# Performance work log

Hardware: AMD Instinct MI355X
Metric: run time of the kernel (lower is better)

The kernel has to match this reference:

```python
import jax, jax.numpy as jnp
import numpy as np

B, S, D = 4, 1024, 4096
HQ, HKV = 32, 8
HD = D // HQ          # 128
SCALE = HQ // HKV     # 4 (GQA repeat factor)


def setup_inputs() -> dict:
    key = jax.random.key(0)
    ks = jax.random.split(key, 11)
    s = 0.02  # init scale for weights
    return {
        "x": jax.random.normal(ks[0], (B, S, D), jnp.float32),
        # freqs_cis stored as (real, imag) pairs: [S, HD//2, 2]
        "freqs_cis": jax.random.normal(ks[1], (S, HD // 2, 2), jnp.float32),
        "Wq": jax.random.normal(ks[2], (D, HQ * HD), jnp.float32) * s,
        "bq": jnp.zeros((HQ * HD,), jnp.float32),
        "Wk": jax.random.normal(ks[3], (D, HKV * HD), jnp.float32) * s,
        "bk": jnp.zeros((HKV * HD,), jnp.float32),
        "Wv": jax.random.normal(ks[4], (D, HKV * HD), jnp.float32) * s,
        "bv": jnp.zeros((HKV * HD,), jnp.float32),
        "Wo": jax.random.normal(ks[5], (D, D), jnp.float32) * s,
        "bo": jnp.zeros((D,), jnp.float32),
        "startpos": 0,
    }


def _apply_rotary(x, fc):
    # x: [B, S, H, HD]; fc: [S, HD//2, 2] (real, imag)
    xr = x.reshape(*x.shape[:-1], HD // 2, 2)
    a, b = xr[..., 0], xr[..., 1]
    c = fc[None, :, None, :, 0]  # [1, S, 1, HD//2]
    d = fc[None, :, None, :, 1]
    # complex multiply (a+ib)*(c+id)
    out = jnp.stack([a * c - b * d, a * d + b * c], axis=-1)
    return out.reshape(x.shape)


def reference(x, freqs_cis, Wq, bq, Wk, bk, Wv, bv, Wo, bo, startpos):
    b, s, _ = x.shape
    q = (x @ Wq + bq).reshape(b, s, HQ, HD)
    k = (x @ Wk + bk).reshape(b, s, HKV, HD)
    v = (x @ Wv + bv).reshape(b, s, HKV, HD)

    fc = freqs_cis[startpos:startpos + s]
    q = _apply_rotary(q, fc)
    k = _apply_rotary(k, fc)

    # startpos == 0 and seq == cache_seq: cache write/read is identity
    q = q.transpose(0, 2, 1, 3)                            # [b, HQ, s, HD]
    k = jnp.repeat(k.transpose(0, 2, 1, 3), SCALE, axis=1)  # GQA repeat -> [b, HQ, s, HD]
    v = jnp.repeat(v.transpose(0, 2, 1, 3), SCALE, axis=1)

    scores = jnp.einsum('bhqd,bhkd->bhqk', q, k) / jnp.sqrt(jnp.float32(HD))
    causal = jnp.tril(jnp.ones((s, s), bool))
    scores = jnp.where(causal, scores, -jnp.inf)
    attn = jax.nn.softmax(scores, axis=-1)
    o = jnp.einsum('bhqk,bhkd->bhqd', attn, v)
    o = o.transpose(0, 2, 1, 3).reshape(b, s, HQ * HD)
    return o @ Wo + bo
```

## Files before the change

kernel.cpp:

```cpp
#include <hip/hip_runtime.h>
#include <hip/hip_bf16.h>

using bf16x8   = __attribute__((ext_vector_type(8))) __bf16;
using floatx4  = __attribute__((ext_vector_type(4))) float;
using floatx16 = __attribute__((ext_vector_type(16))) float;

#define DEVINL __device__ __forceinline__

DEVINL void gload16(const void* g, void* l) {
  __builtin_amdgcn_global_load_lds(
      (__attribute__((address_space(1))) void*)g,
      (__attribute__((address_space(3))) void*)l,
      16, 0, 0);
}

constexpr int S_ = 1024, D_ = 4096, HQ_ = 32, HKV_ = 8, HD_ = 128, B_ = 4;

__global__ void conv_bf16(const float* __restrict__ in, __bf16* __restrict__ out, int n) {
  int i = (blockIdx.x * 256 + threadIdx.x) * 8;
  if (i >= n) return;
  float4 a = *(const float4*)(in + i);
  float4 b = *(const float4*)(in + i + 4);
  bf16x8 o;
  o[0] = (__bf16)a.x; o[1] = (__bf16)a.y; o[2] = (__bf16)a.z; o[3] = (__bf16)a.w;
  o[4] = (__bf16)b.x; o[5] = (__bf16)b.y; o[6] = (__bf16)b.z; o[7] = (__bf16)b.w;
  *(bf16x8*)(out + i) = o;
}

__global__ void conv_transpose(const float* __restrict__ W, __bf16* __restrict__ WT, int K, int N) {
  __shared__ float tile[32][33];
  int n0 = blockIdx.x * 32, k0 = blockIdx.y * 32;
  int tx = threadIdx.x & 31, ty = threadIdx.x >> 5;
#pragma unroll
  for (int i = 0; i < 32; i += 8)
    tile[ty + i][tx] = W[(size_t)(k0 + ty + i) * N + n0 + tx];
  __syncthreads();
#pragma unroll
  for (int i = 0; i < 32; i += 8)
    WT[(size_t)(n0 + ty + i) * K + k0 + tx] = (__bf16)tile[tx][ty + i];
}

template<int MODE>
__global__ __launch_bounds__(512, 2)
void gemm8(const __bf16* __restrict__ A, const __bf16* __restrict__ BT,
           const float* __restrict__ b0, const float* __restrict__ b1,
           const float* __restrict__ b2, void* __restrict__ Cout,
           int M, int N, int K)
{
  __shared__ __bf16 lds[49152];
  const int t = threadIdx.x;
  const int lane = t & 63, w = t >> 6;
  const int wm = w >> 2, wn = w & 3;
  const int g = lane >> 4, c = lane & 15;

  const int gridX = gridDim.x;
  const int nwg = gridDim.x * gridDim.y;
  int lin = blockIdx.y * gridDim.x + blockIdx.x;
  lin = (lin & 7) * (nwg >> 3) + (lin >> 3);
  const int bx = lin % gridX, by = lin / gridX;
  const int m0 = by * 128, n0 = bx * 256;

  const floatx4 zero4 = {0.f, 0.f, 0.f, 0.f};
  floatx4 acc[4][4];
#pragma unroll
  for (int i = 0; i < 4; i++)
#pragma unroll
    for (int j = 0; j < 4; j++) acc[i][j] = zero4;

  const int arow = t >> 2;
  const int achk = (t & 3) ^ ((t >> 3) & 3);
  const __bf16* Ag  = A  + (size_t)(m0 + arow) * K + achk * 8;
  const __bf16* Bg0 = BT + (size_t)(n0 + arow) * K + achk * 8;
  const __bf16* Bg1 = BT + (size_t)(n0 + arow + 128) * K + achk * 8;

  const int sl = (g ^ ((c >> 1) & 3)) * 8;
  const int abase = (wm * 64 + c) * 32 + sl;
  const int bbase = 4096 + (wn * 64 + c) * 32 + sl;

  const int NT = K >> 5;

  auto STAGE = [&](int kt) {
    const int buf = (kt & 3) * 12288;
    const size_t ko = (size_t)kt * 32;
    gload16(Ag  + ko, &lds[buf + t * 8]);
    gload16(Bg0 + ko, &lds[buf + 4096 + t * 8]);
    gload16(Bg1 + ko, &lds[buf + 8192 + t * 8]);
  };

  STAGE(0);
  STAGE(1);
  asm volatile("s_waitcnt vmcnt(3)" ::: "memory");
  __builtin_amdgcn_s_barrier();
  __builtin_amdgcn_sched_barrier(0);

  for (int kt = 0; kt < NT; ++kt) {
    const int buf = (kt & 3) * 12288;
    bf16x8 af[4], bfr[4];
#pragma unroll
    for (int i = 0; i < 4; i++)
      af[i] = *(const bf16x8*)&lds[buf + abase + i * 512];
#pragma unroll
    for (int j = 0; j < 4; j++)
      bfr[j] = *(const bf16x8*)&lds[buf + bbase + j * 512];
    if (kt + 2 < NT) STAGE(kt + 2);
    __builtin_amdgcn_sched_barrier(0);
    __builtin_amdgcn_s_barrier();
    __builtin_amdgcn_sched_barrier(0);
    __builtin_amdgcn_s_setprio(1);
#pragma unroll
    for (int i = 0; i < 4; i++)
#pragma unroll
      for (int j = 0; j < 4; j++)
        acc[i][j] = __builtin_amdgcn_mfma_f32_16x16x32_bf16(af[i], bfr[j], acc[i][j], 0, 0, 0);
    __builtin_amdgcn_s_setprio(0);
    __builtin_amdgcn_sched_barrier(0);
    if (kt + 2 < NT) { asm volatile("s_waitcnt vmcnt(3)" ::: "memory"); }
    else             { asm volatile("s_waitcnt vmcnt(0)" ::: "memory"); }
    __builtin_amdgcn_s_barrier();
    __builtin_amdgcn_sched_barrier(0);
  }

#pragma unroll
  for (int j = 0; j < 4; j++) {
    const int ncol = n0 + wn * 64 + j * 16 + c;
#pragma unroll
    for (int i = 0; i < 4; i++) {
      const int mbase = m0 + wm * 64 + i * 16 + g * 4;
#pragma unroll
      for (int r = 0; r < 4; r++) {
        const int m = mbase + r;
        float v = acc[i][j][r];
        if constexpr (MODE == 0) {
          ((float*)Cout)[(size_t)m * N + ncol] = v + b0[ncol];
        } else {
          const int bb = m >> 10, s = m & 1023;
          __bf16* qkv = (__bf16*)Cout;
          if (ncol < 4096) {
            v += b0[ncol];
            const int h = ncol >> 7, d = ncol & 127;
            qkv[(((size_t)bb * 32 + h) * 1024 + s) * 128 + d] = (__bf16)v;
          } else if (ncol < 5120) {
            const int nc = ncol - 4096;
            v += b1[nc];
            const int h = nc >> 7, d = nc & 127;
            qkv[16777216 + (((size_t)bb * 8 + h) * 1024 + s) * 128 + d] = (__bf16)v;
          } else {
            const int nc = ncol - 5120;
            v += b2[nc];
            const int h = nc >> 7, d = nc & 127;
            qkv[20971520 + (((size_t)bb * 8 + h) * 128 + d) * 1024 + s] = (__bf16)v;
          }
        }
      }
    }
  }
}

constexpr int NQCH = B_ * HQ_ * S_ * (HD_ / 8);
constexpr int NKCH = B_ * HKV_ * S_ * (HD_ / 8);
__global__ void rope_kernel(__bf16* __restrict__ qt, __bf16* __restrict__ kt,
                            const float* __restrict__ fc, const int* __restrict__ sp) {
  int tid = blockIdx.x * 256 + threadIdx.x;
  __bf16* p;
  int idx;
  if (tid < NQCH) { p = qt; idx = tid; }
  else { idx = tid - NQCH; if (idx >= NKCH) return; p = kt; }
  const int c8 = idx & 15;
  const int s  = (idx >> 4) & 1023;
  const int srow = sp[0] + s;
  const float* f = fc + (size_t)srow * 128 + c8 * 8;
  float4 fa = *(const float4*)(f);
  float4 fb = *(const float4*)(f + 4);
  __bf16* q = p + (size_t)idx * 8;
  bf16x8 v = *(const bf16x8*)q;
  float a0 = (float)v[0], b0 = (float)v[1], a1 = (float)v[2], b1 = (float)v[3];
  float a2 = (float)v[4], b2 = (float)v[5], a3 = (float)v[6], b3 = (float)v[7];
  bf16x8 o;
  o[0] = (__bf16)(a0 * fa.x - b0 * fa.y); o[1] = (__bf16)(a0 * fa.y + b0 * fa.x);
  o[2] = (__bf16)(a1 * fa.z - b1 * fa.w); o[3] = (__bf16)(a1 * fa.w + b1 * fa.z);
  o[4] = (__bf16)(a2 * fb.x - b2 * fb.y); o[5] = (__bf16)(a2 * fb.y + b2 * fb.x);
  o[6] = (__bf16)(a3 * fb.z - b3 * fb.w); o[7] = (__bf16)(a3 * fb.w + b3 * fb.z);
  *(bf16x8*)q = o;
}

__global__ __launch_bounds__(256, 2)
void flash_attn(const __bf16* __restrict__ qt, const __bf16* __restrict__ kt,
                const __bf16* __restrict__ vt, __bf16* __restrict__ obuf)
{
  const int lane = threadIdx.x & 63, w = threadIdx.x >> 6;
  const int rl = lane & 31, hi = lane >> 5;
  const int qb = blockIdx.x & 7;
  const int bh = blockIdx.x >> 3;
  const int b = bh >> 5, h = bh & 31, hk = h >> 2;
  const int q0w = (qb + w * 8) * 32;

  const __bf16* Qp = qt + (size_t)(b * HQ_ + h) * S_ * HD_;
  const __bf16* Kp = kt + (size_t)(b * HKV_ + hk) * S_ * HD_;
  const __bf16* Vp = vt + (size_t)(b * HKV_ + hk) * HD_ * S_;

  const __bf16* Qb = Qp + (size_t)(q0w + rl) * HD_ + hi * 8;
  bf16x8 qf[8];
#pragma unroll
  for (int d = 0; d < 8; d++) qf[d] = *(const bf16x8*)(Qb + d * 16);

  const __bf16* Kb = Kp + (size_t)rl * HD_ + hi * 8;
  const __bf16* Vb = Vp + (size_t)rl * S_ + hi * 8;

  const floatx16 zero16 = {0.f,0.f,0.f,0.f,0.f,0.f,0.f,0.f,0.f,0.f,0.f,0.f,0.f,0.f,0.f,0.f};
  floatx16 oacc[4];
#pragma unroll
  for (int dt = 0; dt < 4; dt++) oacc[dt] = zero16;

  float m_run = -__builtin_inff();
  float l_run = 0.f;
  const float ksc = 0.12751744875895f;

  for (int kv0 = 0; kv0 <= q0w; kv0 += 32) {
    floatx16 acc = zero16;
    bf16x8 kf[8];
#pragma unroll
    for (int d = 0; d < 8; d++)
      kf[d] = *(const bf16x8*)(Kb + (size_t)kv0 * HD_ + d * 16);
#pragma unroll
    for (int d = 0; d < 8; d++)
      acc = __builtin_amdgcn_mfma_f32_32x32x16_bf16(kf[d], qf[d], acc, 0, 0, 0);

    bf16x8 vf[4][2];
#pragma unroll
    for (int dt = 0; dt < 4; dt++)
#pragma unroll
      for (int kh = 0; kh < 2; kh++)
        vf[dt][kh] = *(const bf16x8*)(Vb + (size_t)dt * 32 * S_ + kv0 + kh * 16);

    if (kv0 == q0w) {
#pragma unroll
      for (int r = 0; r < 16; r++) {
        const int krel = (r & 3) + 8 * (r >> 2) + 4 * hi;
        if (krel > rl) acc[r] = -3e29f;
      }
    }

    float mx = acc[0];
#pragma unroll
    for (int r = 1; r < 16; r++) mx = fmaxf(mx, acc[r]);
    mx = fmaxf(mx, __shfl_xor(mx, 32));
    const float m_cand = mx * ksc;

    float m_use;
    const bool defer = __all(m_cand - m_run <= 8.0f);
    if (defer) {
      m_use = m_run;
    } else {
      const float m_new = fmaxf(m_run, m_cand);
      const float alpha = exp2f(m_run - m_new);
      l_run *= alpha;
      float ar[16];
#pragma unroll
      for (int r = 0; r < 16; r++)
        ar[r] = __shfl(alpha, (r & 3) + 8 * (r >> 2) + 4 * hi);
#pragma unroll
      for (int dt = 0; dt < 4; dt++)
#pragma unroll
        for (int r = 0; r < 16; r++) oacc[dt][r] *= ar[r];
      m_run = m_new;
      m_use = m_new;
    }

    float pr[16];
#pragma unroll
    for (int r = 0; r < 16; r++) pr[r] = exp2f(fmaf(acc[r], ksc, -m_use));
    float rs = pr[0];
#pragma unroll
    for (int r = 1; r < 16; r++) rs += pr[r];
    rs += __shfl_xor(rs, 32);
    l_run += rs;

    bf16x8 pa[2];
#pragma unroll
    for (int kh = 0; kh < 2; kh++) {
      const int rb = kh * 8;
      unsigned a0, b0, a1, b1;
      asm("v_cvt_pk_bf16_f32 %0, %1, %2" : "=v"(a0) : "v"(pr[rb + 0]), "v"(pr[rb + 1]));
      asm("v_cvt_pk_bf16_f32 %0, %1, %2" : "=v"(b0) : "v"(pr[rb + 4]), "v"(pr[rb + 5]));
      asm("v_cvt_pk_bf16_f32 %0, %1, %2" : "=v"(a1) : "v"(pr[rb + 2]), "v"(pr[rb + 3]));
      asm("v_cvt_pk_bf16_f32 %0, %1, %2" : "=v"(b1) : "v"(pr[rb + 6]), "v"(pr[rb + 7]));
      asm("v_permlane32_swap_b32 %0, %1" : "+v"(a0), "+v"(b0));
      asm("v_permlane32_swap_b32 %0, %1" : "+v"(a1), "+v"(b1));
      union { unsigned u[4]; bf16x8 v; } cvt;
      cvt.u[0] = a0; cvt.u[1] = a1; cvt.u[2] = b0; cvt.u[3] = b1;
      pa[kh] = cvt.v;
    }

#pragma unroll
    for (int dt = 0; dt < 4; dt++) {
      oacc[dt] = __builtin_amdgcn_mfma_f32_32x32x16_bf16(pa[0], vf[dt][0], oacc[dt], 0, 0, 0);
      oacc[dt] = __builtin_amdgcn_mfma_f32_32x32x16_bf16(pa[1], vf[dt][1], oacc[dt], 0, 0, 0);
    }
  }

  const float linv = 1.f / l_run;
  float lr[16];
#pragma unroll
  for (int r = 0; r < 16; r++)
    lr[r] = __shfl(linv, (r & 3) + 8 * (r >> 2) + 4 * hi);
#pragma unroll
  for (int dt = 0; dt < 4; dt++)
#pragma unroll
    for (int r = 0; r < 16; r++) {
      const int qrow = q0w + (r & 3) + 8 * (r >> 2) + 4 * hi;
      const size_t o = (size_t)(b * S_ + qrow) * D_ + h * HD_ + dt * 32 + rl;
      obuf[o] = (__bf16)(oacc[dt][r] * lr[r]);
    }
}

extern "C" void kernel_launch(void* const* d_in, const int* in_sizes, int n_in,
                              void* d_out, int out_size, void* d_ws, size_t ws_size,
                              hipStream_t stream) {
  (void)in_sizes; (void)n_in; (void)out_size;
  const float* x  = (const float*)d_in[0];
  const float* fc = (const float*)d_in[1];
  const float* Wq = (const float*)d_in[2];
  const float* bq = (const float*)d_in[3];
  const float* Wk = (const float*)d_in[4];
  const float* bk = (const float*)d_in[5];
  const float* Wv = (const float*)d_in[6];
  const float* bv = (const float*)d_in[7];
  const float* Wo = (const float*)d_in[8];
  const float* bo = (const float*)d_in[9];
  const int*   sp = (const int*)d_in[10];
  float* out = (float*)d_out;

  const size_t MB = 1024 * 1024;
  if (ws_size < 192 * MB) return;
  char* ws = (char*)d_ws;
  __bf16* xb     = (__bf16*)(ws + 0);
  __bf16* WqkvT  = (__bf16*)(ws + 32 * MB);
  __bf16* WoT    = (__bf16*)(ws + 80 * MB);
  __bf16* q_t    = (__bf16*)(ws + 112 * MB);
  __bf16* k_t    = (__bf16*)(ws + 144 * MB);
  __bf16* v_t    = (__bf16*)(ws + 152 * MB);
  __bf16* ob     = (__bf16*)(ws + 160 * MB);

  conv_bf16<<<8192, 256, 0, stream>>>(x, xb, D_ * B_ * S_);
  conv_transpose<<<dim3(128, 128), 256, 0, stream>>>(Wq, WqkvT, 4096, 4096);
  conv_transpose<<<dim3(32, 128),  256, 0, stream>>>(Wk, WqkvT + (size_t)4096 * 4096, 4096, 1024);
  conv_transpose<<<dim3(32, 128),  256, 0, stream>>>(Wv, WqkvT + (size_t)5120 * 4096, 4096, 1024);
  conv_transpose<<<dim3(128, 128), 256, 0, stream>>>(Wo, WoT, 4096, 4096);

  gemm8<1><<<dim3(24, 32), 512, 0, stream>>>(xb, WqkvT, bq, bk, bv, q_t, 4096, 6144, 4096);

  rope_kernel<<<(NQCH + NKCH) / 256, 256, 0, stream>>>(q_t, k_t, fc, sp);
  flash_attn<<<1024, 256, 0, stream>>>(q_t, k_t, v_t, ob);

  gemm8<0><<<dim3(16, 32), 512, 0, stream>>>(ob, WoT, bo, nullptr, nullptr, out, 4096, 4096, 4096);
}
```

Before: 664.3 us.

## Enlarge GEMM tiles to 256x256 with quadrant-pipelined double-buffered K=64 loads

Replaces the 128x256 GEMM with a 256x256 tile kernel using BK=64 and two LDS buffers. Each K step is split into four quadrant phases, each staging one 128-row sub-tile of the next stage while MFMAs run on the current one, with staggered vmcnt waits. The larger tile raises arithmetic intensity per global byte. In exchange it uses 128KB of LDS per block, which limits occupancy, and it halves the grid: 384 and 256 blocks spread across the device's CUs.

```diff
diff --git a/kernel.cpp b/kernel.cpp
--- a/kernel.cpp
+++ b/kernel.cpp
@@ -42,118 +42,170 @@
 
 template<int MODE>
 __global__ __launch_bounds__(512, 2)
-void gemm8(const __bf16* __restrict__ A, const __bf16* __restrict__ BT,
-           const float* __restrict__ b0, const float* __restrict__ b1,
-           const float* __restrict__ b2, void* __restrict__ Cout,
-           int M, int N, int K)
+void gemm8p(const __bf16* __restrict__ A, const __bf16* __restrict__ BT,
+            const float* __restrict__ b0, const float* __restrict__ b1,
+            const float* __restrict__ b2, void* __restrict__ Cout,
+            int M, int N, int K)
 {
-  __shared__ __bf16 lds[49152];
+  __shared__ __bf16 lds[65536];
   const int t = threadIdx.x;
   const int lane = t & 63, w = t >> 6;
   const int wm = w >> 2, wn = w & 3;
-  const int g = lane >> 4, c = lane & 15;
+  const int g = (lane >> 4) & 3, c = lane & 15;
 
   const int gridX = gridDim.x;
   const int nwg = gridDim.x * gridDim.y;
   int lin = blockIdx.y * gridDim.x + blockIdx.x;
   lin = (lin & 7) * (nwg >> 3) + (lin >> 3);
   const int bx = lin % gridX, by = lin / gridX;
-  const int m0 = by * 128, n0 = bx * 256;
+  const int m0 = by * 256, n0 = bx * 256;
 
   const floatx4 zero4 = {0.f, 0.f, 0.f, 0.f};
-  floatx4 acc[4][4];
-#pragma unroll
-  for (int i = 0; i < 4; i++)
-#pragma unroll
-    for (int j = 0; j < 4; j++) acc[i][j] = zero4;
-
-  const int arow = t >> 2;
-  const int achk = (t & 3) ^ ((t >> 3) & 3);
-  const __bf16* Ag  = A  + (size_t)(m0 + arow) * K + achk * 8;
-  const __bf16* Bg0 = BT + (size_t)(n0 + arow) * K + achk * 8;
-  const __bf16* Bg1 = BT + (size_t)(n0 + arow + 128) * K + achk * 8;
-
-  const int sl = (g ^ ((c >> 1) & 3)) * 8;
-  const int abase = (wm * 64 + c) * 32 + sl;
-  const int bbase = 4096 + (wn * 64 + c) * 32 + sl;
-
-  const int NT = K >> 5;
-
-  auto STAGE = [&](int kt) {
-    const int buf = (kt & 3) * 12288;
-    const size_t ko = (size_t)kt * 32;
-    gload16(Ag  + ko, &lds[buf + t * 8]);
-    gload16(Bg0 + ko, &lds[buf + 4096 + t * 8]);
-    gload16(Bg1 + ko, &lds[buf + 8192 + t * 8]);
-  };
-
-  STAGE(0);
-  STAGE(1);
-  asm volatile("s_waitcnt vmcnt(3)" ::: "memory");
-  __builtin_amdgcn_s_barrier();
+  floatx4 acc[2][2][4][2];
+#pragma unroll
+  for (int a = 0; a < 2; a++)
+#pragma unroll
+    for (int bq = 0; bq < 2; bq++)
+#pragma unroll
+      for (int i = 0; i < 4; i++)
+#pragma unroll
+        for (int j = 0; j < 2; j++) acc[a][bq][i][j] = zero4;
+
+  const int t3 = t >> 3;
+  const int l8 = ((t & 7) ^ (t3 & 7)) * 8;
+  const int browc = (t3 & 31) + ((t3 >> 5) << 6);
+  const __bf16* srcA0 = A  + (size_t)(m0 + t3) * K + l8;
+  const __bf16* srcA1 = A  + (size_t)(m0 + 64 + t3) * K + l8;
+  const __bf16* srcB0 = BT + (size_t)(n0 + browc) * K + l8;
+  const __bf16* srcB1 = BT + (size_t)(n0 + 32 + browc) * K + l8;
+  const size_t k128 = (size_t)128 * K;
+
+  const int arow_rd = (wm * 64 + c) * 64;
+  const int brow_rd = (wn * 32 + c) * 64;
+  const int sel0 = ((g) ^ (c & 7)) * 8;
+  const int sel1 = ((4 + g) ^ (c & 7)) * 8;
+
+  const int NT = K >> 6;
+
+#define STG(srcp, subofs, kt, pbuf)                                              \
+  gload16((srcp) + (size_t)(kt) * 64,        &lds[(pbuf) + (subofs) + t * 8]);   \
+  gload16((srcp) + (size_t)(kt) * 64 + k128, &lds[(pbuf) + (subofs) + 4096 + t * 8]);
+
+#define LOADA(MQ, bb)                                                            \
+  _Pragma("unroll")                                                              \
+  for (int i = 0; i < 4; i++) {                                                  \
+    af[i][0] = *(const bf16x8*)&lds[(bb) + (MQ)*8192 + arow_rd + i*1024 + sel0]; \
+    af[i][1] = *(const bf16x8*)&lds[(bb) + (MQ)*8192 + arow_rd + i*1024 + sel1]; \
+  }
+
+#define LOADB(NQ, bb)                                                            \
+  _Pragma("unroll")                                                              \
+  for (int j = 0; j < 2; j++) {                                                  \
+    bf[j][0] = *(const bf16x8*)&lds[(bb) + 16384 + (NQ)*8192 + brow_rd + j*1024 + sel0]; \
+    bf[j][1] = *(const bf16x8*)&lds[(bb) + 16384 + (NQ)*8192 + brow_rd + j*1024 + sel1]; \
+  }
+
+#define MFMAQ(MQ, NQ)                                                            \
+  __builtin_amdgcn_s_setprio(1);                                                 \
+  _Pragma("unroll")                                                              \
+  for (int i = 0; i < 4; i++)                                                    \
+    _Pragma("unroll")                                                            \
+    for (int j = 0; j < 2; j++) {                                                \
+      acc[MQ][NQ][i][j] = __builtin_amdgcn_mfma_f32_16x16x32_bf16(af[i][0], bf[j][0], acc[MQ][NQ][i][j], 0, 0, 0); \
+      acc[MQ][NQ][i][j] = __builtin_amdgcn_mfma_f32_16x16x32_bf16(af[i][1], bf[j][1], acc[MQ][NQ][i][j], 0, 0, 0); \
+    }                                                                            \
+  __builtin_amdgcn_s_setprio(0);                                                 \
   __builtin_amdgcn_sched_barrier(0);
 
-  for (int kt = 0; kt < NT; ++kt) {
-    const int buf = (kt & 3) * 12288;
-    bf16x8 af[4], bfr[4];
-#pragma unroll
-    for (int i = 0; i < 4; i++)
-      af[i] = *(const bf16x8*)&lds[buf + abase + i * 512];
-#pragma unroll
-    for (int j = 0; j < 4; j++)
-      bfr[j] = *(const bf16x8*)&lds[buf + bbase + j * 512];
-    if (kt + 2 < NT) STAGE(kt + 2);
-    __builtin_amdgcn_sched_barrier(0);
-    __builtin_amdgcn_s_barrier();
-    __builtin_amdgcn_sched_barrier(0);
-    __builtin_amdgcn_s_setprio(1);
-#pragma unroll
-    for (int i = 0; i < 4; i++)
-#pragma unroll
-      for (int j = 0; j < 4; j++)
-        acc[i][j] = __builtin_amdgcn_mfma_f32_16x16x32_bf16(af[i], bfr[j], acc[i][j], 0, 0, 0);
-    __builtin_amdgcn_s_setprio(0);
-    __builtin_amdgcn_sched_barrier(0);
-    if (kt + 2 < NT) { asm volatile("s_waitcnt vmcnt(3)" ::: "memory"); }
-    else             { asm volatile("s_waitcnt vmcnt(0)" ::: "memory"); }
-    __builtin_amdgcn_s_barrier();
-    __builtin_amdgcn_sched_barrier(0);
+#define BAR()                                                                    \
+  __builtin_amdgcn_sched_barrier(0);                                             \
+  __builtin_amdgcn_s_barrier();                                                  \
+  __builtin_amdgcn_sched_barrier(0);
+
+#define VMC(N) asm volatile("s_waitcnt vmcnt(" #N ")" ::: "memory");
+
+#define TILE(v, DOSTAGE, VM0, VM1, VM2) {                                        \
+  const int bb = ((v) & 1) * 32768;                                              \
+  const int nb = bb ^ 32768;                                                     \
+  bf16x8 af[4][2], bf[2][2];                                                     \
+                                                                         \
+  if (DOSTAGE) { STG(srcA0, 0, (v) + 1, nb) }                                    \
+  VMC(VM0) BAR()                                                                 \
+  LOADA(0, bb) LOADB(0, bb)                                                      \
+  MFMAQ(0, 0)                                                                    \
+                                                                         \
+  if (DOSTAGE) { STG(srcB0, 16384, (v) + 1, nb) }                                \
+  VMC(VM1) BAR()                                                                 \
+  LOADB(1, bb)                                                                   \
+  MFMAQ(0, 1)                                                                    \
+                                                                         \
+  if (DOSTAGE) { STG(srcB1, 24576, (v) + 1, nb) }                                \
+  VMC(VM2) BAR()                                                                 \
+  LOADA(1, bb)                                                                   \
+  MFMAQ(1, 1)                                                                    \
+                                                                         \
+  if (DOSTAGE) { STG(srcA1, 8192, (v) + 1, nb) }                                 \
+  BAR()                                                                          \
+  LOADB(0, bb)                                                                   \
+  MFMAQ(1, 0)                                                                    \
+}
+
+  STG(srcA0, 0, 0, 0)
+  STG(srcB0, 16384, 0, 0)
+  STG(srcB1, 24576, 0, 0)
+  STG(srcA1, 8192, 0, 0)
+
+  for (int v = 0; v < NT - 1; ++v) {
+    TILE(v, true, 6, 6, 6)
   }
-
-#pragma unroll
-  for (int j = 0; j < 4; j++) {
-    const int ncol = n0 + wn * 64 + j * 16 + c;
-#pragma unroll
-    for (int i = 0; i < 4; i++) {
-      const int mbase = m0 + wm * 64 + i * 16 + g * 4;
-#pragma unroll
-      for (int r = 0; r < 4; r++) {
-        const int m = mbase + r;
-        float v = acc[i][j][r];
-        if constexpr (MODE == 0) {
-          ((float*)Cout)[(size_t)m * N + ncol] = v + b0[ncol];
-        } else {
-          const int bb = m >> 10, s = m & 1023;
-          __bf16* qkv = (__bf16*)Cout;
-          if (ncol < 4096) {
-            v += b0[ncol];
-            const int h = ncol >> 7, d = ncol & 127;
-            qkv[(((size_t)bb * 32 + h) * 1024 + s) * 128 + d] = (__bf16)v;
-          } else if (ncol < 5120) {
-            const int nc = ncol - 4096;
-            v += b1[nc];
-            const int h = nc >> 7, d = nc & 127;
-            qkv[16777216 + (((size_t)bb * 8 + h) * 1024 + s) * 128 + d] = (__bf16)v;
-          } else {
-            const int nc = ncol - 5120;
-            v += b2[nc];
-            const int h = nc >> 7, d = nc & 127;
-            qkv[20971520 + (((size_t)bb * 8 + h) * 128 + d) * 1024 + s] = (__bf16)v;
+  TILE(NT - 1, false, 4, 2, 0)
+
+#undef STG
+#undef LOADA
+#undef LOADB
+#undef MFMAQ
+#undef BAR
+#undef VMC
+#undef TILE
+
+#pragma unroll
+  for (int mq = 0; mq < 2; mq++)
+#pragma unroll
+    for (int nq = 0; nq < 2; nq++)
+#pragma unroll
+      for (int j = 0; j < 2; j++) {
+        const int ncol = n0 + wn * 64 + nq * 32 + j * 16 + c;
+#pragma unroll
+        for (int i = 0; i < 4; i++) {
+          const int mbase = m0 + wm * 128 + mq * 64 + i * 16 + g * 4;
+#pragma unroll
+          for (int r = 0; r < 4; r++) {
+            const int m = mbase + r;
+            float v = acc[mq][nq][i][j][r];
+            if constexpr (MODE == 0) {
+              ((float*)Cout)[(size_t)m * N + ncol] = v + b0[ncol];
+            } else {
+              const int bb2 = m >> 10, s = m & 1023;
+              __bf16* qkv = (__bf16*)Cout;
+              if (ncol < 4096) {
+                v += b0[ncol];
+                const int h = ncol >> 7, d = ncol & 127;
+                qkv[(((size_t)bb2 * 32 + h) * 1024 + s) * 128 + d] = (__bf16)v;
+              } else if (ncol < 5120) {
+                const int nc = ncol - 4096;
+                v += b1[nc];
+                const int h = nc >> 7, d = nc & 127;
+                qkv[16777216 + (((size_t)bb2 * 8 + h) * 1024 + s) * 128 + d] = (__bf16)v;
+              } else {
+                const int nc = ncol - 5120;
+                v += b2[nc];
+                const int h = nc >> 7, d = nc & 127;
+                qkv[20971520 + (((size_t)bb2 * 8 + h) * 128 + d) * 1024 + s] = (__bf16)v;
+              }
+            }
           }
         }
       }
-    }
-  }
 }
 
 constexpr int NQCH = B_ * HQ_ * S_ * (HD_ / 8);
@@ -347,10 +399,10 @@
   conv_transpose<<<dim3(32, 128),  256, 0, stream>>>(Wv, WqkvT + (size_t)5120 * 4096, 4096, 1024);
   conv_transpose<<<dim3(128, 128), 256, 0, stream>>>(Wo, WoT, 4096, 4096);
 
-  gemm8<1><<<dim3(24, 32), 512, 0, stream>>>(xb, WqkvT, bq, bk, bv, q_t, 4096, 6144, 4096);
+  gemm8p<1><<<dim3(24, 16), 512, 0, stream>>>(xb, WqkvT, bq, bk, bv, q_t, 4096, 6144, 4096);
 
   rope_kernel<<<(NQCH + NKCH) / 256, 256, 0, stream>>>(q_t, k_t, fc, sp);
   flash_attn<<<1024, 256, 0, stream>>>(q_t, k_t, v_t, ob);
 
-  gemm8<0><<<dim3(16, 32), 512, 0, stream>>>(ob, WoT, bo, nullptr, nullptr, out, 4096, 4096, 4096);
-}
+  gemm8p<0><<<dim3(16, 16), 512, 0, stream>>>(ob, WoT, bo, nullptr, nullptr, out, 4096, 4096, 4096);
+}
```

New measurement: 617.8 us. 1.08x faster.
